# Performance work log

Measured on AMD Instinct MI355X. Metric: run time of the kernel, lower is better.

## Reference

```python
import jax, jax.numpy as jnp
import numpy as np
from jax import lax

B, T0, H0, W0 = 8, 8, 14, 14
C, NH = 768, 8
D = C // NH            # head_dim = 96
N = T0 * H0 * W0 + 1   # 1569 tokens incl. cls
SCALE = D ** -0.5
EPS = 1e-5


def _pool_norm(xh, conv_w, ln_g, ln_b, thw, stride):
    """AttentionPool with depthwise conv3d + LayerNorm. xh: [B, NH, N, D]."""
    cls_tok, xs = xh[:, :, :1, :], xh[:, :, 1:, :]
    b, n, _, d = xs.shape
    t, h, w = thw
    # (b n) c t h w
    xs = xs.reshape(b * n, t, h, w, d).transpose(0, 4, 1, 2, 3)
    y = lax.conv_general_dilated(
        xs, conv_w, window_strides=stride,
        padding=[(1, 1), (1, 1), (1, 1)],
        feature_group_count=d,
        dimension_numbers=("NCDHW", "OIDHW", "NCDHW"))
    ot, oh, ow = y.shape[2], y.shape[3], y.shape[4]
    y = y.transpose(0, 2, 3, 4, 1).reshape(b, n, ot * oh * ow, d)
    y = jnp.concatenate([cls_tok, y], axis=2)
    mu = y.mean(-1, keepdims=True)
    var = y.var(-1, keepdims=True)
    y = (y - mu) * lax.rsqrt(var + EPS) * ln_g + ln_b
    return y, (ot, oh, ow)


def setup_inputs() -> dict:
    key = jax.random.key(0)
    ks = jax.random.split(key, 12)
    s = lambda fan: (1.0 / np.sqrt(fan))
    return {
        "x": jax.random.normal(ks[0], (B, N, C), jnp.float32),
        "W_qkv": jax.random.normal(ks[1], (C, 3 * C), jnp.float32) * s(C),
        "b_qkv": jnp.zeros((3 * C,), jnp.float32),
        "W_proj": jax.random.normal(ks[2], (C, C), jnp.float32) * s(C),
        "b_proj": jnp.zeros((C,), jnp.float32),
        "conv_q_w": jax.random.normal(ks[3], (D, 1, 3, 3, 3), jnp.float32) * s(27),
        "conv_k_w": jax.random.normal(ks[4], (D, 1, 3, 3, 3), jnp.float32) * s(27),
        "conv_v_w": jax.random.normal(ks[5], (D, 1, 3, 3, 3), jnp.float32) * s(27),
        "lnq_g": jnp.ones((D,), jnp.float32), "lnq_b": jnp.zeros((D,), jnp.float32),
        "lnk_g": jnp.ones((D,), jnp.float32), "lnk_b": jnp.zeros((D,), jnp.float32),
        "lnv_g": jnp.ones((D,), jnp.float32), "lnv_b": jnp.zeros((D,), jnp.float32),
        "t": T0, "h": H0, "w": W0,
    }


def reference(x, W_qkv, b_qkv, W_proj, b_proj,
              conv_q_w, conv_k_w, conv_v_w,
              lnq_g, lnq_b, lnk_g, lnk_b, lnv_g, lnv_b,
              t, h, w):
    thw = (int(t), int(h), int(w))
    Bx, Nx, Cx = x.shape
    qkv = x @ W_qkv + b_qkv                       # [B, N, 3C]
    qkv = qkv.reshape(Bx, Nx, 3, NH, D).transpose(2, 0, 3, 1, 4)  # qkv b h n d
    q, k, v = qkv[0], qkv[1], qkv[2]
    q, q_shape = _pool_norm(q, conv_q_w, lnq_g, lnq_b, thw, (1, 1, 1))
    k, _ = _pool_norm(k, conv_k_w, lnk_g, lnk_b, thw, (1, 2, 2))
    v, _ = _pool_norm(v, conv_v_w, lnv_g, lnv_b, thw, (1, 2, 2))
    dots = jnp.einsum("bhid,bhjd->bhij", q, k) * SCALE
    attn = jax.nn.softmax(dots, axis=-1)
    out = jnp.einsum("bhij,bhjd->bhid", attn, v)  # [B, NH, Nq, D]
    out = out.transpose(0, 2, 1, 3).reshape(Bx, -1, Cx)
    out = out @ W_proj + b_proj
    return out
```

## Files before the change

### kernel.cpp

```cpp
#include <hip/hip_runtime.h>
#include <hip/hip_bf16.h>
#include <math.h>

#define B_   8
#define NH_  8
#define D_   96
#define C_   768
#define N_   1569
#define NKV_ 393
#define M_   (B_*N_)
#define QKV1 ((size_t)B_*NH_*N_*D_)
#define QPAD 1664
#define KPAD 416
#define SCALE_ 0.10206207261596575f

using short8v = __attribute__((ext_vector_type(8))) short;
using f32x4   = __attribute__((ext_vector_type(4))) float;
using f32x2   = __attribute__((ext_vector_type(2))) float;
typedef unsigned short u16;

#define GLOAD_LDS16(g, l) __builtin_amdgcn_global_load_lds( \
    (const __attribute__((address_space(1))) void*)(g),     \
    (__attribute__((address_space(3))) void*)(l), 16, 0, 0)

static __device__ __forceinline__ u16 f2bf(float f) {
    __hip_bfloat16 b = __float2bfloat16(f);
    return *(u16*)&b;
}

static __device__ __forceinline__ unsigned xcd_swizzle(unsigned orig, unsigned nwg) {
    const unsigned qq = nwg >> 3, rr = nwg & 7;
    const unsigned xcd = orig & 7, loc = orig >> 3;
    return (xcd < rr ? xcd * (qq + 1) : rr * (qq + 1) + (xcd - rr) * qq) + loc;
}

#define PREP_CVT_B   9414
#define PREP_WQ_B    1728
#define PREP_WP_B    576
#define PREP_WT_B    31
#define PREP_ZP_B    552
#define PREP_BLOCKS  (PREP_CVT_B + PREP_WQ_B + PREP_WP_B + PREP_WT_B + PREP_ZP_B)

static __device__ __forceinline__
void tile_transpose(const float* __restrict__ W, u16* __restrict__ Wt,
                    int ncols, int n0, int k0, float* tile )
{
    const int tx = threadIdx.x & 31, ty = threadIdx.x >> 5;
    #pragma unroll
    for (int i = 0; i < 4; ++i)
        tile[(ty + i * 8) * 33 + tx] = W[(size_t)(k0 + ty + i * 8) * ncols + n0 + tx];
    __syncthreads();
    #pragma unroll
    for (int i = 0; i < 4; ++i)
        Wt[(size_t)(n0 + ty + i * 8) * 768 + k0 + tx] = f2bf(tile[tx * 33 + ty + i * 8]);
}

__global__ __launch_bounds__(256)
void prep_kernel(const float* __restrict__ x, const float* __restrict__ Wqkv,
                 const float* __restrict__ Wproj,
                 const float* __restrict__ cwq, const float* __restrict__ cwk,
                 const float* __restrict__ cwv,
                 u16* __restrict__ x16, u16* __restrict__ Wqkvt,
                 u16* __restrict__ Wprojt, float* __restrict__ cwT,
                 u16* __restrict__ vt16)
{
    __shared__ float tile[32 * 33];
    const int bid = blockIdx.x;
    const int tid = threadIdx.x;

    if (bid < PREP_CVT_B) {
        const int i = bid * 256 + tid;
        const int n4 = M_ * 768 / 4;
        if (i < n4) {
            const float4 v = ((const float4*)x)[i];
            ushort4 o;
            o.x = f2bf(v.x); o.y = f2bf(v.y); o.z = f2bf(v.z); o.w = f2bf(v.w);
            ((ushort4*)x16)[i] = o;
        }
    } else if (bid < PREP_CVT_B + PREP_WQ_B) {
        const int b2 = bid - PREP_CVT_B;
        tile_transpose(Wqkv, Wqkvt, 2304, (b2 % 72) * 32, (b2 / 72) * 32, tile);
    } else if (bid < PREP_CVT_B + PREP_WQ_B + PREP_WP_B) {
        const int b2 = bid - PREP_CVT_B - PREP_WQ_B;
        tile_transpose(Wproj, Wprojt, 768, (b2 % 24) * 32, (b2 / 24) * 32, tile);
    } else if (bid < PREP_CVT_B + PREP_WQ_B + PREP_WP_B + PREP_WT_B) {
        const int i = (bid - PREP_CVT_B - PREP_WQ_B - PREP_WP_B) * 256 + tid;
        if (i < 3 * 27 * 96) {
            const int tsr = i / 2592;
            const int r = i - tsr * 2592;
            const int tap = r / 96, ch = r - tap * 96;
            const float* src = tsr == 0 ? cwq : (tsr == 1 ? cwk : cwv);
            cwT[i] = src[ch * 27 + tap];
        }
    } else {
        const int i = (bid - PREP_CVT_B - PREP_WQ_B - PREP_WP_B - PREP_WT_B) * 256 + tid;
        const int total = 64 * 96 * (KPAD - NKV_);
        if (i < total) {
            const int j = i % (KPAD - NKV_);
            const int rest = i / (KPAD - NKV_);
            vt16[(size_t)rest * KPAD + NKV_ + j] = 0;
        }
    }
}

template<int NC, bool SCATTER>
__global__ __launch_bounds__(512)
void gemm_bf16_kernel(const u16* __restrict__ A, const u16* __restrict__ Bt,
                      const float* __restrict__ bias, void* __restrict__ outp)
{
    constexpr int NXT = NC / 128;
    __shared__ alignas(16) u16 As[2][128 * 64];
    __shared__ alignas(16) u16 Bs[2][128 * 64];

    const int tid  = threadIdx.x;
    const int w    = tid >> 6, lane = tid & 63;
    const int c    = lane & 15, g = lane >> 4;
    const int wm   = w >> 2, wn = w & 3;
    const int lrow = lane >> 3, lcol = lane & 7;

    const unsigned wg = xcd_swizzle(blockIdx.x, gridDim.x);
    const int m0 = (int)(wg / NXT) * 128;
    const int n0 = (int)(wg % NXT) * 128;

    f32x4 acc[4][2];
    #pragma unroll
    for (int i = 0; i < 4; ++i)
        #pragma unroll
        for (int j = 0; j < 2; ++j) acc[i][j] = (f32x4){0.f, 0.f, 0.f, 0.f};

#define STAGE(BUF, K0) do {                                                      \
    _Pragma("unroll")                                                            \
    for (int t = 0; t < 2; ++t) {                                                \
        const int r = t * 64 + w * 8;                                            \
        const int row = r + lrow;                                                \
        const int scol = (lcol ^ (row & 7)) * 8;                                 \
        int m = m0 + row; if (m >= M_) m = M_ - 1;                               \
        GLOAD_LDS16(&A[(size_t)m * 768 + (K0) + scol], &As[BUF][r * 64]);        \
        GLOAD_LDS16(&Bt[(size_t)(n0 + row) * 768 + (K0) + scol],                 \
                    &Bs[BUF][r * 64]);                                           \
    } } while (0)

    const int xora = (g ^ (c & 7)) * 8;
    const int xorb = ((4 + g) ^ (c & 7)) * 8;

#define KSTEP(BUF, LAST, PREF, KNEXT) do {                                       \
    if (LAST) asm volatile("s_waitcnt vmcnt(0)" ::: "memory");                   \
    else      asm volatile("s_waitcnt vmcnt(4)" ::: "memory");                   \
    __builtin_amdgcn_s_barrier();                                                \
    short8v a0[4], a1[4], b0[2], b1[2];                                          \
    _Pragma("unroll")                                                            \
    for (int i = 0; i < 4; ++i) {                                                \
        const int ra = (wm * 64 + i * 16 + c) * 64;                              \
        a0[i] = *(const short8v*)&As[BUF][ra + xora];                            \
        a1[i] = *(const short8v*)&As[BUF][ra + xorb];                            \
    }                                                                            \
    _Pragma("unroll")                                                            \
    for (int j = 0; j < 2; ++j) {                                                \
        const int rb = (wn * 32 + j * 16 + c) * 64;                              \
        b0[j] = *(const short8v*)&Bs[BUF][rb + xora];                            \
        b1[j] = *(const short8v*)&Bs[BUF][rb + xorb];                            \
    }                                                                            \
    asm volatile("s_waitcnt lgkmcnt(0)" ::: "memory");                           \
    __builtin_amdgcn_sched_barrier(0);                                           \
    __builtin_amdgcn_s_barrier();                                                \
    if (PREF) STAGE(BUF, KNEXT);                                                 \
    __builtin_amdgcn_s_setprio(1);                                               \
    _Pragma("unroll")                                                            \
    for (int i = 0; i < 4; ++i)                                                  \
        _Pragma("unroll")                                                        \
        for (int j = 0; j < 2; ++j)                                              \
            acc[i][j] = __builtin_amdgcn_mfma_f32_16x16x32_bf16(                 \
                a0[i], b0[j], acc[i][j], 0, 0, 0);                               \
    _Pragma("unroll")                                                            \
    for (int i = 0; i < 4; ++i)                                                  \
        _Pragma("unroll")                                                        \
        for (int j = 0; j < 2; ++j)                                              \
            acc[i][j] = __builtin_amdgcn_mfma_f32_16x16x32_bf16(                 \
                a1[i], b1[j], acc[i][j], 0, 0, 0);                               \
    __builtin_amdgcn_s_setprio(0);                                               \
    } while (0)

    STAGE(0, 0);
    STAGE(1, 64);
    #pragma unroll
    for (int tt = 0; tt < 5; ++tt) {
        KSTEP(0, false, true, (2 * tt + 2) * 64);
        KSTEP(1, false, true, (2 * tt + 3) * 64);
    }
    KSTEP(0, false, false, 0);
    KSTEP(1, true,  false, 0);
#undef STAGE
#undef KSTEP

    #pragma unroll
    for (int i = 0; i < 4; ++i) {
        const int mrow = m0 + wm * 64 + i * 16 + g * 4;
        #pragma unroll
        for (int j = 0; j < 2; ++j) {
            const int ncol = n0 + wn * 32 + j * 16 + c;
            const float bv = bias[ncol];
            if constexpr (SCATTER) {
                u16* out = (u16*)outp;
                const int s   = ncol / C_;
                const int rem = ncol - s * C_;
                const int hh  = rem / D_;
                const int dd  = rem - hh * D_;
                #pragma unroll
                for (int r = 0; r < 4; ++r) {
                    const int m = mrow + r;
                    if (m < M_) {
                        const int bb2 = m / N_;
                        const int n = m - bb2 * N_;
                        out[(size_t)s * QKV1 +
                            ((size_t)(bb2 * NH_ + hh) * N_ + n) * D_ + dd] = f2bf(acc[i][j][r] + bv);
                    }
                }
            } else {
                float* out = (float*)outp;
                #pragma unroll
                for (int r = 0; r < 4; ++r) {
                    const int m = mrow + r;
                    if (m < M_) out[(size_t)m * NC + ncol] = acc[i][j][r] + bv;
                }
            }
        }
    }
}

static __device__ __forceinline__ void loadx6(const u16* __restrict__ rowp,
                                              int iw, f32x2 x[3])
{
    if (iw < 0 || iw >= 14) {
        x[0] = x[1] = x[2] = (f32x2){0.f, 0.f};
        return;
    }
    const unsigned* p = (const unsigned*)(rowp + (size_t)iw * 96);
    #pragma unroll
    for (int j = 0; j < 3; ++j) {
        const unsigned u = p[j];
        x[j][0] = __uint_as_float(u << 16);
        x[j][1] = __uint_as_float(u & 0xffff0000u);
    }
}

template<int STRIDE, int OHW, int WMODE, int WO0>
static __device__ __forceinline__
void pool_task(const u16* __restrict__ in, const float* __restrict__ cwT,
               const float* __restrict__ g, const float* __restrict__ bta,
               u16* __restrict__ out, int tokstride, int bh, int to, int ho,
               float oscale)
{
    const int sl = threadIdx.x & 15;
    const u16* base = in + (size_t)bh * N_ * 96 + 6 * sl;

    f32x2 acc[7][3];
    #pragma unroll
    for (int i = 0; i < 7; ++i)
        #pragma unroll
        for (int p = 0; p < 3; ++p) acc[i][p] = (f32x2){0.f, 0.f};

    #pragma unroll
    for (int dt = 0; dt < 3; ++dt) {
        const int t = to - 1 + dt;
        if (t < 0 || t > 7) continue;
        #pragma unroll
        for (int dh = 0; dh < 3; ++dh) {
            const int h = ho * STRIDE - 1 + dh;
            if (h < 0 || h >= 14) continue;
            const int tapb = dt * 9 + dh * 3;
            f32x2 wt[3][3];
            #pragma unroll
            for (int dw = 0; dw < 3; ++dw)
                #pragma unroll
                for (int p = 0; p < 3; ++p)
                    wt[dw][p] = *(const f32x2*)&cwT[(tapb + dw) * 96 + 6 * sl + 2 * p];
            const u16* rowp = base + (size_t)(1 + t * 196 + h * 14) * 96;

            if constexpr (STRIDE == 1) {
                f32x2 xm[3], x0[3], xp[3];
                loadx6(rowp, WO0 - 1, xm);
                loadx6(rowp, WO0, x0);
                #pragma unroll
                for (int wo = 0; wo < 7; ++wo) {
                    loadx6(rowp, WO0 + wo + 1, xp);
                    #pragma unroll
                    for (int p = 0; p < 3; ++p) {
                        acc[wo][p] = __builtin_elementwise_fma(wt[0][p], xm[p], acc[wo][p]);
                        acc[wo][p] = __builtin_elementwise_fma(wt[1][p], x0[p], acc[wo][p]);
                        acc[wo][p] = __builtin_elementwise_fma(wt[2][p], xp[p], acc[wo][p]);
                        xm[p] = x0[p]; x0[p] = xp[p];
                    }
                }
            } else {
                #pragma unroll
                for (int wo = 0; wo < 7; ++wo) {
                    #pragma unroll
                    for (int dw = 0; dw < 3; ++dw) {
                        f32x2 xa[3];
                        loadx6(rowp, 2 * wo - 1 + dw, xa);
                        #pragma unroll
                        for (int p = 0; p < 3; ++p)
                            acc[wo][p] = __builtin_elementwise_fma(wt[dw][p], xa[p], acc[wo][p]);
                    }
                }
            }
        }
    }

    f32x2 gg[3], bb[3];
    #pragma unroll
    for (int p = 0; p < 3; ++p) {
        gg[p] = *(const f32x2*)&g[6 * sl + 2 * p] * oscale;
        bb[p] = *(const f32x2*)&bta[6 * sl + 2 * p] * oscale;
    }

    #pragma unroll
    for (int wo = 0; wo < 7; ++wo) {
        float s = acc[wo][0][0] + acc[wo][0][1] + acc[wo][1][0] + acc[wo][1][1]
                + acc[wo][2][0] + acc[wo][2][1];
        float sq = acc[wo][0][0] * acc[wo][0][0];
        sq = fmaf(acc[wo][0][1], acc[wo][0][1], sq);
        sq = fmaf(acc[wo][1][0], acc[wo][1][0], sq);
        sq = fmaf(acc[wo][1][1], acc[wo][1][1], sq);
        sq = fmaf(acc[wo][2][0], acc[wo][2][0], sq);
        sq = fmaf(acc[wo][2][1], acc[wo][2][1], sq);
        #pragma unroll
        for (int off = 1; off < 16; off <<= 1) {
            s  += __shfl_xor(s, off, 64);
            sq += __shfl_xor(sq, off, 64);
        }
        const float mu = s * (1.f / 96.f);
        const float rstd = rsqrtf(sq * (1.f / 96.f) - mu * mu + 1e-5f);
        const f32x2 muv = (f32x2){mu, mu};
        const int tok = 1 + (to * OHW + ho) * OHW + WO0 + wo;
        u16 yb[6];
        #pragma unroll
        for (int p = 0; p < 3; ++p) {
            const f32x2 y = (acc[wo][p] - muv) * rstd * gg[p] + bb[p];
            yb[2 * p] = f2bf(y[0]); yb[2 * p + 1] = f2bf(y[1]);
        }
        if constexpr (WMODE == 2) {
            #pragma unroll
            for (int j = 0; j < 6; ++j)
                out[((size_t)bh * 96 + 6 * sl + j) * KPAD + tok] = yb[j];
        } else {
            unsigned* op = (unsigned*)&out[((size_t)bh * tokstride + tok) * 96 + 6 * sl];
            #pragma unroll
            for (int p = 0; p < 3; ++p)
                op[p] = (unsigned)yb[2 * p] | ((unsigned)yb[2 * p + 1] << 16);
        }
    }
}

template<int WMODE>
static __device__ __forceinline__
void pool_cls_v5(const u16* __restrict__ in, const float* __restrict__ g,
                 const float* __restrict__ bta, u16* __restrict__ out,
                 int tokstride, int bh, float oscale)
{
    const int sl = threadIdx.x & 15;
    const unsigned* p = (const unsigned*)(in + (size_t)bh * N_ * 96 + 6 * sl);
    f32x2 v[3];
    #pragma unroll
    for (int j = 0; j < 3; ++j) {
        const unsigned u = p[j];
        v[j][0] = __uint_as_float(u << 16);
        v[j][1] = __uint_as_float(u & 0xffff0000u);
    }
    float s = v[0][0] + v[0][1] + v[1][0] + v[1][1] + v[2][0] + v[2][1];
    float sq = v[0][0]*v[0][0] + v[0][1]*v[0][1] + v[1][0]*v[1][0]
             + v[1][1]*v[1][1] + v[2][0]*v[2][0] + v[2][1]*v[2][1];
    #pragma unroll
    for (int off = 1; off < 16; off <<= 1) {
        s  += __shfl_xor(s, off, 64);
        sq += __shfl_xor(sq, off, 64);
    }
    const float mu = s * (1.f / 96.f);
    const float rstd = rsqrtf(sq * (1.f / 96.f) - mu * mu + 1e-5f);
    u16 yb[6];
    #pragma unroll
    for (int p2 = 0; p2 < 3; ++p2) {
        const f32x2 gg = *(const f32x2*)&g[6 * sl + 2 * p2] * oscale;
        const f32x2 bb = *(const f32x2*)&bta[6 * sl + 2 * p2] * oscale;
        const f32x2 y = (v[p2] - (f32x2){mu, mu}) * rstd * gg + bb;
        yb[2 * p2] = f2bf(y[0]); yb[2 * p2 + 1] = f2bf(y[1]);
    }
    if constexpr (WMODE == 2) {
        #pragma unroll
        for (int j = 0; j < 6; ++j)
            out[((size_t)bh * 96 + 6 * sl + j) * KPAD] = yb[j];
    } else {
        unsigned* op = (unsigned*)&out[(size_t)bh * tokstride * 96 + 6 * sl];
        #pragma unroll
        for (int p2 = 0; p2 < 3; ++p2)
            op[p2] = (unsigned)yb[2 * p2] | ((unsigned)yb[2 * p2 + 1] << 16);
    }
}

#define NTASKS 21696
__global__ __launch_bounds__(256)
void pool_ln_v5_kernel(const u16* __restrict__ qin, const u16* __restrict__ kin,
                       const u16* __restrict__ vin, const float* __restrict__ cwT,
                       const float* __restrict__ gq, const float* __restrict__ bq,
                       const float* __restrict__ gk, const float* __restrict__ bk,
                       const float* __restrict__ gv, const float* __restrict__ bv,
                       u16* __restrict__ qout, u16* __restrict__ kout,
                       u16* __restrict__ vtout)
{
    const unsigned wg = xcd_swizzle(blockIdx.x, gridDim.x);
    const int gid = (int)(wg * 16 + (threadIdx.x >> 4));
    if (gid >= NTASKS) return;

    if (gid < 14336) {
        const int chunk = gid / 7168;
        const int r = gid - chunk * 7168;
        const int ho = r % 14;
        const int to = (r / 14) & 7;
        const int bh = r / 112;
        if (chunk == 0)
            pool_task<1, 14, 0, 0>(qin, cwT, gq, bq, qout, QPAD, bh, to, ho, SCALE_);
        else
            pool_task<1, 14, 0, 7>(qin, cwT, gq, bq, qout, QPAD, bh, to, ho, SCALE_);
    } else if (gid < 17920) {
        const int r = gid - 14336;
        const int ho = r % 7;
        const int to = (r / 7) & 7;
        const int bh = r / 56;
        pool_task<2, 7, 0, 0>(kin, cwT + 2592, gk, bk, kout, KPAD, bh, to, ho, 1.f);
    } else if (gid < 21504) {
        const int r = gid - 17920;
        const int ho = r % 7;
        const int to = (r / 7) & 7;
        const int bh = r / 56;
        pool_task<2, 7, 2, 0>(vin, cwT + 5184, gv, bv, vtout, KPAD, bh, to, ho, 1.f);
    } else {
        const int r = gid - 21504;
        const int tsr = r >> 6, bh = r & 63;
        if (tsr == 0)      pool_cls_v5<0>(qin, gq, bq, qout, QPAD, bh, SCALE_);
        else if (tsr == 1) pool_cls_v5<0>(kin, gk, bk, kout, KPAD, bh, 1.f);
        else               pool_cls_v5<2>(vin, gv, bv, vtout, KPAD, bh, 1.f);
    }
}

__global__ __launch_bounds__(256)
void attn_mfma_kernel(const u16* __restrict__ Q, const u16* __restrict__ K,
                      const u16* __restrict__ VT, u16* __restrict__ Out)
{
    __shared__ alignas(16) u16 plds[4][2][512];
    const int tid  = threadIdx.x;
    const int w    = tid >> 6, lane = tid & 63;
    const int c    = lane & 15, g = lane >> 4;

    const unsigned wg = xcd_swizzle(blockIdx.x, gridDim.x);
    const int bh = (int)(wg / 13);
    const int b  = bh >> 3, hh = bh & 7;
    const int q0 = (int)(wg % 13) * 128 + w * 32;

    const size_t qbase = (size_t)bh * QPAD * 96;
    const size_t kbase = (size_t)bh * KPAD * 96;

    short8v qa[2][3];
    #pragma unroll
    for (int s2 = 0; s2 < 2; ++s2)
        #pragma unroll
        for (int kf = 0; kf < 3; ++kf)
            qa[s2][kf] = *(const short8v*)
                &Q[qbase + (size_t)(q0 + s2 * 16 + c) * 96 + kf * 32 + g * 8];

    f32x4 oacc[2][6];
    #pragma unroll
    for (int s2 = 0; s2 < 2; ++s2)
        #pragma unroll
        for (int t = 0; t < 6; ++t) oacc[s2][t] = (f32x4){0.f, 0.f, 0.f, 0.f};
    float lsum[2][4] = {{0.f,0.f,0.f,0.f},{0.f,0.f,0.f,0.f}};

    short8v kb[2][6];
#define LOADK(IDX, PR) do {                                                     \
    _Pragma("unroll")                                                           \
    for (int h = 0; h < 2; ++h)                                                 \
        _Pragma("unroll")                                                       \
        for (int kf = 0; kf < 3; ++kf)                                          \
            kb[IDX][h * 3 + kf] = *(const short8v*)                             \
                &K[kbase + (size_t)((PR) * 32 + h * 16 + c) * 96 + kf * 32 + g * 8]; \
    } while (0)

    LOADK(0, 0);

    #pragma unroll
    for (int pr = 0; pr < 13; ++pr) {
        const int cur = pr & 1, nxt = cur ^ 1;

        short8v vt[6];
        #pragma unroll
        for (int t = 0; t < 6; ++t)
            vt[t] = *(const short8v*)
                &VT[kbase + (size_t)(t * 16 + c) * KPAD + pr * 32 + g * 8];

        f32x4 sacc[2][2];
        __builtin_amdgcn_s_setprio(1);
        #pragma unroll
        for (int s2 = 0; s2 < 2; ++s2)
            #pragma unroll
            for (int h = 0; h < 2; ++h) {
                f32x4 sa = (f32x4){0.f, 0.f, 0.f, 0.f};
                sa = __builtin_amdgcn_mfma_f32_16x16x32_bf16(qa[s2][0], kb[cur][h*3+0], sa, 0, 0, 0);
                sa = __builtin_amdgcn_mfma_f32_16x16x32_bf16(qa[s2][1], kb[cur][h*3+1], sa, 0, 0, 0);
                sa = __builtin_amdgcn_mfma_f32_16x16x32_bf16(qa[s2][2], kb[cur][h*3+2], sa, 0, 0, 0);
                sacc[s2][h] = sa;
            }
        __builtin_amdgcn_s_setprio(0);

        if (pr < 12) LOADK(nxt, pr + 1);

        #pragma unroll
        for (int h = 0; h < 2; ++h) {
            const int jcol = pr * 32 + h * 16 + c;
            #pragma unroll
            for (int r = 0; r < 4; ++r) {
                float s = sacc[0][h][r];
                if (jcol >= NKV_) s = -1e30f;
                const float p = __expf(s);
                lsum[0][r] += p;
                const int q    = g * 4 + r;
                const int j    = h * 16 + c;
                const int dstL = q | ((j >> 3) << 4);
                plds[w][0][dstL * 8 + (j & 7)] = f2bf(p);
            }
        }
        asm volatile("s_waitcnt lgkmcnt(0)" ::: "memory");
        __builtin_amdgcn_sched_barrier(0);
        {
            const short8v pa0 = *(const short8v*)&plds[w][0][lane * 8];
            __builtin_amdgcn_s_setprio(1);
            #pragma unroll
            for (int t = 0; t < 6; ++t)
                oacc[0][t] = __builtin_amdgcn_mfma_f32_16x16x32_bf16(pa0, vt[t], oacc[0][t], 0, 0, 0);
            __builtin_amdgcn_s_setprio(0);
        }

        #pragma unroll
        for (int h = 0; h < 2; ++h) {
            const int jcol = pr * 32 + h * 16 + c;
            #pragma unroll
            for (int r = 0; r < 4; ++r) {
                float s = sacc[1][h][r];
                if (jcol >= NKV_) s = -1e30f;
                const float p = __expf(s);
                lsum[1][r] += p;
                const int q    = g * 4 + r;
                const int j    = h * 16 + c;
                const int dstL = q | ((j >> 3) << 4);
                plds[w][1][dstL * 8 + (j & 7)] = f2bf(p);
            }
        }
        asm volatile("s_waitcnt lgkmcnt(0)" ::: "memory");
        __builtin_amdgcn_sched_barrier(0);
        {
            const short8v pa1 = *(const short8v*)&plds[w][1][lane * 8];
            __builtin_amdgcn_s_setprio(1);
            #pragma unroll
            for (int t = 0; t < 6; ++t)
                oacc[1][t] = __builtin_amdgcn_mfma_f32_16x16x32_bf16(pa1, vt[t], oacc[1][t], 0, 0, 0);
            __builtin_amdgcn_s_setprio(0);
        }
    }
#undef LOADK

    float linv[2][4];
    #pragma unroll
    for (int s2 = 0; s2 < 2; ++s2)
        #pragma unroll
        for (int r = 0; r < 4; ++r) {
            float s = lsum[s2][r];
            s += __shfl_xor(s, 1, 64);
            s += __shfl_xor(s, 2, 64);
            s += __shfl_xor(s, 4, 64);
            s += __shfl_xor(s, 8, 64);
            linv[s2][r] = 1.f / s;
        }

    #pragma unroll
    for (int s2 = 0; s2 < 2; ++s2)
        #pragma unroll
        for (int t = 0; t < 6; ++t)
            #pragma unroll
            for (int r = 0; r < 4; ++r) {
                const int row = q0 + s2 * 16 + g * 4 + r;
                if (row < N_)
                    Out[((size_t)(b * N_ + row)) * 768 + hh * 96 + t * 16 + c] =
                        f2bf(oacc[s2][t][r] * linv[s2][r]);
            }
}

extern "C" void kernel_launch(void* const* d_in, const int* in_sizes, int n_in,
                              void* d_out, int out_size, void* d_ws, size_t ws_size,
                              hipStream_t stream)
{
    const float* x     = (const float*)d_in[0];
    const float* Wqkv  = (const float*)d_in[1];
    const float* bqkv  = (const float*)d_in[2];
    const float* Wproj = (const float*)d_in[3];
    const float* bproj = (const float*)d_in[4];
    const float* cwq   = (const float*)d_in[5];
    const float* cwk   = (const float*)d_in[6];
    const float* cwv   = (const float*)d_in[7];
    const float* lnqg  = (const float*)d_in[8];
    const float* lnqb  = (const float*)d_in[9];
    const float* lnkg  = (const float*)d_in[10];
    const float* lnkb  = (const float*)d_in[11];
    const float* lnvg  = (const float*)d_in[12];
    const float* lnvb  = (const float*)d_in[13];

    u16* ws = (u16*)d_ws;
    u16* qkv_raw = ws;
    u16* q16 = qkv_raw + 3 * QKV1;
    u16* k16 = q16 + (size_t)64 * QPAD * 96;
    u16* vt16 = k16 + (size_t)64 * KPAD * 96;
    u16* x16    = vt16 + (size_t)64 * KPAD * 96;
    u16* Wqkvt  = x16 + (size_t)M_ * 768;
    u16* Wprojt = Wqkvt + (size_t)2304 * 768;
    float* cwT  = (float*)(Wprojt + (size_t)768 * 768);
    u16* attn16 = qkv_raw;
    float* out = (float*)d_out;

    prep_kernel<<<PREP_BLOCKS, 256, 0, stream>>>(
        x, Wqkv, Wproj, cwq, cwk, cwv, x16, Wqkvt, Wprojt, cwT, vt16);

    gemm_bf16_kernel<2304, true><<<18 * 99, 512, 0, stream>>>(x16, Wqkvt, bqkv, qkv_raw);

    pool_ln_v5_kernel<<<(NTASKS + 15) / 16, 256, 0, stream>>>(
        qkv_raw, qkv_raw + QKV1, qkv_raw + 2 * QKV1, cwT,
        lnqg, lnqb, lnkg, lnkb, lnvg, lnvb, q16, k16, vt16);

    attn_mfma_kernel<<<13 * 64, 256, 0, stream>>>(q16, k16, vt16, attn16);

    gemm_bf16_kernel<768, false><<<6 * 99, 512, 0, stream>>>(attn16, Wprojt, bproj, out);
}
```

Baseline: 199.2 us.

## Widen GEMM tile to 128x256 with single-buffered LDS

Both GEMMs now use 128x256 output tiles instead of 128x128, so each wave computes a 64x64 sub-tile with 16 accumulators, halving the grid size. The LDS double buffer is dropped in favour of a single buffer. The next K-slice is prefetched after the first half-step's reads and a full vmcnt(0) wait precedes each step. This aims to raise arithmetic intensity and cut A-tile reloads, at the cost of exposed load latency, more registers, and fewer blocks (297 for the projection GEMM), which may underfill the GPU.

Result: faster. 190.0 us (-4.6%).

```diff
diff --git a/kernel.cpp b/kernel.cpp
--- a/kernel.cpp
+++ b/kernel.cpp
@@ -104,13 +104,13 @@
 }
 
 template<int NC, bool SCATTER>
-__global__ __launch_bounds__(512)
+__global__ __launch_bounds__(512, 4)
 void gemm_bf16_kernel(const u16* __restrict__ A, const u16* __restrict__ Bt,
                       const float* __restrict__ bias, void* __restrict__ outp)
 {
-    constexpr int NXT = NC / 128;
-    __shared__ alignas(16) u16 As[2][128 * 64];
-    __shared__ alignas(16) u16 Bs[2][128 * 64];
+    constexpr int NXT = NC / 256;
+    __shared__ alignas(16) u16 As[128 * 64];
+    __shared__ alignas(16) u16 Bs[256 * 64];
 
     const int tid  = threadIdx.x;
     const int w    = tid >> 6, lane = tid & 63;
@@ -120,75 +120,81 @@
 
     const unsigned wg = xcd_swizzle(blockIdx.x, gridDim.x);
     const int m0 = (int)(wg / NXT) * 128;
-    const int n0 = (int)(wg % NXT) * 128;
-
-    f32x4 acc[4][2];
+    const int n0 = (int)(wg % NXT) * 256;
+
+    f32x4 acc[4][4];
     #pragma unroll
     for (int i = 0; i < 4; ++i)
         #pragma unroll
-        for (int j = 0; j < 2; ++j) acc[i][j] = (f32x4){0.f, 0.f, 0.f, 0.f};
-
-#define STAGE(BUF, K0) do {                                                      \
+        for (int j = 0; j < 4; ++j) acc[i][j] = (f32x4){0.f, 0.f, 0.f, 0.f};
+
+#define STAGE(K0) do {                                                           \
     _Pragma("unroll")                                                            \
-    for (int t = 0; t < 2; ++t) {                                                \
-        const int r = t * 64 + w * 8;                                            \
-        const int row = r + lrow;                                                \
+    for (int it2 = 0; it2 < 2; ++it2) {                                          \
+        const int rb = it2 * 64 + w * 8;                                         \
+        const int row = rb + lrow;                                               \
         const int scol = (lcol ^ (row & 7)) * 8;                                 \
         int m = m0 + row; if (m >= M_) m = M_ - 1;                               \
-        GLOAD_LDS16(&A[(size_t)m * 768 + (K0) + scol], &As[BUF][r * 64]);        \
-        GLOAD_LDS16(&Bt[(size_t)(n0 + row) * 768 + (K0) + scol],                 \
-                    &Bs[BUF][r * 64]);                                           \
+        GLOAD_LDS16(&A[(size_t)m * 768 + (K0) + scol], &As[rb * 64]);            \
+    }                                                                            \
+    _Pragma("unroll")                                                            \
+    for (int it2 = 0; it2 < 4; ++it2) {                                          \
+        const int rb = it2 * 64 + w * 8;                                         \
+        const int row = rb + lrow;                                               \
+        const int scol = (lcol ^ (row & 7)) * 8;                                 \
+        GLOAD_LDS16(&Bt[(size_t)(n0 + row) * 768 + (K0) + scol], &Bs[rb * 64]);  \
     } } while (0)
 
     const int xora = (g ^ (c & 7)) * 8;
     const int xorb = ((4 + g) ^ (c & 7)) * 8;
 
-#define KSTEP(BUF, LAST, PREF, KNEXT) do {                                       \
-    if (LAST) asm volatile("s_waitcnt vmcnt(0)" ::: "memory");                   \
-    else      asm volatile("s_waitcnt vmcnt(4)" ::: "memory");                   \
+#define KSTEP(T) do {                                                            \
+    asm volatile("s_waitcnt vmcnt(0)" ::: "memory");                             \
     __builtin_amdgcn_s_barrier();                                                \
-    short8v a0[4], a1[4], b0[2], b1[2];                                          \
-    _Pragma("unroll")                                                            \
-    for (int i = 0; i < 4; ++i) {                                                \
-        const int ra = (wm * 64 + i * 16 + c) * 64;                              \
-        a0[i] = *(const short8v*)&As[BUF][ra + xora];                            \
-        a1[i] = *(const short8v*)&As[BUF][ra + xorb];                            \
+    {                                                                            \
+        short8v a0[4], b0[4];                                                    \
+        _Pragma("unroll")                                                        \
+        for (int i = 0; i < 4; ++i)                                              \
+            a0[i] = *(const short8v*)&As[(wm * 64 + i * 16 + c) * 64 + xora];    \
+        _Pragma("unroll")                                                        \
+        for (int j = 0; j < 4; ++j)                                              \
+            b0[j] = *(const short8v*)&Bs[(wn * 64 + j * 16 + c) * 64 + xora];    \
+        asm volatile("s_waitcnt lgkmcnt(0)" ::: "memory");                       \
+        __builtin_amdgcn_sched_barrier(0);                                       \
+        __builtin_amdgcn_s_setprio(1);                                           \
+        _Pragma("unroll")                                                        \
+        for (int i = 0; i < 4; ++i)                                              \
+            _Pragma("unroll")                                                    \
+            for (int j = 0; j < 4; ++j)                                          \
+                acc[i][j] = __builtin_amdgcn_mfma_f32_16x16x32_bf16(             \
+                    a0[i], b0[j], acc[i][j], 0, 0, 0);                           \
+        __builtin_amdgcn_s_setprio(0);                                           \
     }                                                                            \
-    _Pragma("unroll")                                                            \
-    for (int j = 0; j < 2; ++j) {                                                \
-        const int rb = (wn * 32 + j * 16 + c) * 64;                              \
-        b0[j] = *(const short8v*)&Bs[BUF][rb + xora];                            \
-        b1[j] = *(const short8v*)&Bs[BUF][rb + xorb];                            \
-    }                                                                            \
-    asm volatile("s_waitcnt lgkmcnt(0)" ::: "memory");                           \
-    __builtin_amdgcn_sched_barrier(0);                                           \
-    __builtin_amdgcn_s_barrier();                                                \
-    if (PREF) STAGE(BUF, KNEXT);                                                 \
-    __builtin_amdgcn_s_setprio(1);                                               \
-    _Pragma("unroll")                                                            \
-    for (int i = 0; i < 4; ++i)                                                  \
+    {                                                                            \
+        short8v a1[4], b1[4];                                                    \
         _Pragma("unroll")                                                        \
-        for (int j = 0; j < 2; ++j)                                              \
-            acc[i][j] = __builtin_amdgcn_mfma_f32_16x16x32_bf16(                 \
-                a0[i], b0[j], acc[i][j], 0, 0, 0);                               \
-    _Pragma("unroll")                                                            \
-    for (int i = 0; i < 4; ++i)                                                  \
+        for (int i = 0; i < 4; ++i)                                              \
+            a1[i] = *(const short8v*)&As[(wm * 64 + i * 16 + c) * 64 + xorb];    \
         _Pragma("unroll")                                                        \
-        for (int j = 0; j < 2; ++j)                                              \
-            acc[i][j] = __builtin_amdgcn_mfma_f32_16x16x32_bf16(                 \
-                a1[i], b1[j], acc[i][j], 0, 0, 0);                               \
-    __builtin_amdgcn_s_setprio(0);                                               \
-    } while (0)
-
-    STAGE(0, 0);
-    STAGE(1, 64);
-    #pragma unroll
-    for (int tt = 0; tt < 5; ++tt) {
-        KSTEP(0, false, true, (2 * tt + 2) * 64);
-        KSTEP(1, false, true, (2 * tt + 3) * 64);
-    }
-    KSTEP(0, false, false, 0);
-    KSTEP(1, true,  false, 0);
+        for (int j = 0; j < 4; ++j)                                              \
+            b1[j] = *(const short8v*)&Bs[(wn * 64 + j * 16 + c) * 64 + xorb];    \
+        asm volatile("s_waitcnt lgkmcnt(0)" ::: "memory");                       \
+        __builtin_amdgcn_sched_barrier(0);                                       \
+        __builtin_amdgcn_s_barrier();                                            \
+        if ((T) + 1 < 12) STAGE(((T) + 1) * 64);                                 \
+        __builtin_amdgcn_s_setprio(1);                                           \
+        _Pragma("unroll")                                                        \
+        for (int i = 0; i < 4; ++i)                                              \
+            _Pragma("unroll")                                                    \
+            for (int j = 0; j < 4; ++j)                                          \
+                acc[i][j] = __builtin_amdgcn_mfma_f32_16x16x32_bf16(             \
+                    a1[i], b1[j], acc[i][j], 0, 0, 0);                           \
+        __builtin_amdgcn_s_setprio(0);                                           \
+    } } while (0)
+
+    STAGE(0);
+    #pragma unroll
+    for (int t = 0; t < 12; ++t) KSTEP(t);
 #undef STAGE
 #undef KSTEP
 
@@ -196,8 +202,8 @@
     for (int i = 0; i < 4; ++i) {
         const int mrow = m0 + wm * 64 + i * 16 + g * 4;
         #pragma unroll
-        for (int j = 0; j < 2; ++j) {
-            const int ncol = n0 + wn * 32 + j * 16 + c;
+        for (int j = 0; j < 4; ++j) {
+            const int ncol = n0 + wn * 64 + j * 16 + c;
             const float bv = bias[ncol];
             if constexpr (SCATTER) {
                 u16* out = (u16*)outp;
@@ -626,7 +632,7 @@
     prep_kernel<<<PREP_BLOCKS, 256, 0, stream>>>(
         x, Wqkv, Wproj, cwq, cwk, cwv, x16, Wqkvt, Wprojt, cwT, vt16);
 
-    gemm_bf16_kernel<2304, true><<<18 * 99, 512, 0, stream>>>(x16, Wqkvt, bqkv, qkv_raw);
+    gemm_bf16_kernel<2304, true><<<99 * 9, 512, 0, stream>>>(x16, Wqkvt, bqkv, qkv_raw);
 
     pool_ln_v5_kernel<<<(NTASKS + 15) / 16, 256, 0, stream>>>(
         qkv_raw, qkv_raw + QKV1, qkv_raw + 2 * QKV1, cwT,
@@ -634,5 +640,5 @@
 
     attn_mfma_kernel<<<13 * 64, 256, 0, stream>>>(q16, k16, vt16, attn16);
 
-    gemm_bf16_kernel<768, false><<<6 * 99, 512, 0, stream>>>(attn16, Wprojt, bproj, out);
-}
+    gemm_bf16_kernel<768, false><<<99 * 3, 512, 0, stream>>>(attn16, Wprojt, bproj, out);
+}
```

## Single-buffer GEMM LDS with split-phase prefetch and wider N tile for QKV

Applied to the files above, without the earlier changes.

Restructures the bf16 GEMM from a double-buffered LDS pipeline to a single buffer. The next K-tile load is issued mid-step, after the fragment reads into registers, and overlaps with the second half of the MFMAs. It also adds a templated N tile, so the QKV projection uses 256-wide tiles with half as many blocks, and sets a launch-bounds occupancy hint. The aim is to cut LDS footprint for higher occupancy and to reuse A tiles across more columns, at the cost of extra barriers and less prefetch distance per step.

Result: slower. 298.9 us (+50.1%).

```diff
diff --git a/kernel.cpp b/kernel.cpp
--- a/kernel.cpp
+++ b/kernel.cpp
@@ -103,14 +103,21 @@
     }
 }
 
-template<int NC, bool SCATTER>
-__global__ __launch_bounds__(512)
+#define WAIT_VM(n)  asm volatile("s_waitcnt vmcnt(" #n ")" ::: "memory")
+#define WAIT_LG(n)  asm volatile("s_waitcnt lgkmcnt(" #n ")" ::: "memory")
+
+template<int NC, int BN, bool SCATTER>
+__global__ __launch_bounds__(512, 4)
 void gemm_bf16_kernel(const u16* __restrict__ A, const u16* __restrict__ Bt,
                       const float* __restrict__ bias, void* __restrict__ outp)
 {
-    constexpr int NXT = NC / 128;
-    __shared__ alignas(16) u16 As[2][128 * 64];
-    __shared__ alignas(16) u16 Bs[2][128 * 64];
+    constexpr int NXT    = NC / BN;
+    constexpr int WN     = BN / 4;
+    constexpr int NBF    = WN / 16;
+    constexpr int BLOADS = BN / 64;
+
+    __shared__ alignas(16) u16 As[128 * 64];
+    __shared__ alignas(16) u16 Bs[BN * 64];
 
     const int tid  = threadIdx.x;
     const int w    = tid >> 6, lane = tid & 63;
@@ -120,75 +127,81 @@
 
     const unsigned wg = xcd_swizzle(blockIdx.x, gridDim.x);
     const int m0 = (int)(wg / NXT) * 128;
-    const int n0 = (int)(wg % NXT) * 128;
-
-    f32x4 acc[4][2];
+    const int n0 = (int)(wg % NXT) * BN;
+
+    f32x4 acc[4][NBF];
     #pragma unroll
     for (int i = 0; i < 4; ++i)
         #pragma unroll
-        for (int j = 0; j < 2; ++j) acc[i][j] = (f32x4){0.f, 0.f, 0.f, 0.f};
-
-#define STAGE(BUF, K0) do {                                                      \
+        for (int j = 0; j < NBF; ++j) acc[i][j] = (f32x4){0.f, 0.f, 0.f, 0.f};
+
+#define STAGE(K0) do {                                                           \
     _Pragma("unroll")                                                            \
-    for (int t = 0; t < 2; ++t) {                                                \
-        const int r = t * 64 + w * 8;                                            \
-        const int row = r + lrow;                                                \
+    for (int it2 = 0; it2 < 2; ++it2) {                                          \
+        const int rb = it2 * 64 + w * 8;                                         \
+        const int row = rb + lrow;                                               \
         const int scol = (lcol ^ (row & 7)) * 8;                                 \
         int m = m0 + row; if (m >= M_) m = M_ - 1;                               \
-        GLOAD_LDS16(&A[(size_t)m * 768 + (K0) + scol], &As[BUF][r * 64]);        \
-        GLOAD_LDS16(&Bt[(size_t)(n0 + row) * 768 + (K0) + scol],                 \
-                    &Bs[BUF][r * 64]);                                           \
+        GLOAD_LDS16(&A[(size_t)m * 768 + (K0) + scol], &As[rb * 64]);            \
+    }                                                                            \
+    _Pragma("unroll")                                                            \
+    for (int it2 = 0; it2 < BLOADS; ++it2) {                                     \
+        const int rb = it2 * 64 + w * 8;                                         \
+        const int row = rb + lrow;                                               \
+        const int scol = (lcol ^ (row & 7)) * 8;                                 \
+        GLOAD_LDS16(&Bt[(size_t)(n0 + row) * 768 + (K0) + scol], &Bs[rb * 64]);  \
     } } while (0)
 
     const int xora = (g ^ (c & 7)) * 8;
     const int xorb = ((4 + g) ^ (c & 7)) * 8;
 
-#define KSTEP(BUF, LAST, PREF, KNEXT) do {                                       \
-    if (LAST) asm volatile("s_waitcnt vmcnt(0)" ::: "memory");                   \
-    else      asm volatile("s_waitcnt vmcnt(4)" ::: "memory");                   \
+#define KSTEP(T) do {                                                            \
+          \
+    if constexpr (BLOADS == 4) WAIT_VM(4); else WAIT_VM(2);                      \
     __builtin_amdgcn_s_barrier();                                                \
-    short8v a0[4], a1[4], b0[2], b1[2];                                          \
+    short8v a0[4], a1[4], b0[NBF], b1[NBF];                                      \
     _Pragma("unroll")                                                            \
     for (int i = 0; i < 4; ++i) {                                                \
         const int ra = (wm * 64 + i * 16 + c) * 64;                              \
-        a0[i] = *(const short8v*)&As[BUF][ra + xora];                            \
-        a1[i] = *(const short8v*)&As[BUF][ra + xorb];                            \
+        a0[i] = *(const short8v*)&As[ra + xora];                                 \
+        a1[i] = *(const short8v*)&As[ra + xorb];                                 \
     }                                                                            \
+                                  \
+    WAIT_VM(0);                                                                  \
+    __builtin_amdgcn_s_barrier();                                                \
     _Pragma("unroll")                                                            \
-    for (int j = 0; j < 2; ++j) {                                                \
-        const int rb = (wn * 32 + j * 16 + c) * 64;                              \
-        b0[j] = *(const short8v*)&Bs[BUF][rb + xora];                            \
-        b1[j] = *(const short8v*)&Bs[BUF][rb + xorb];                            \
+    for (int j = 0; j < NBF; ++j) {                                              \
+        const int rb = (wn * WN + j * 16 + c) * 64;                              \
+        b0[j] = *(const short8v*)&Bs[rb + xora];                                 \
+        b1[j] = *(const short8v*)&Bs[rb + xorb];                                 \
     }                                                                            \
-    asm volatile("s_waitcnt lgkmcnt(0)" ::: "memory");                           \
+    if constexpr (NBF == 4) WAIT_LG(4); else WAIT_LG(2);                         \
     __builtin_amdgcn_sched_barrier(0);                                           \
-    __builtin_amdgcn_s_barrier();                                                \
-    if (PREF) STAGE(BUF, KNEXT);                                                 \
     __builtin_amdgcn_s_setprio(1);                                               \
     _Pragma("unroll")                                                            \
     for (int i = 0; i < 4; ++i)                                                  \
         _Pragma("unroll")                                                        \
-        for (int j = 0; j < 2; ++j)                                              \
+        for (int j = 0; j < NBF; ++j)                                            \
             acc[i][j] = __builtin_amdgcn_mfma_f32_16x16x32_bf16(                 \
                 a0[i], b0[j], acc[i][j], 0, 0, 0);                               \
+    __builtin_amdgcn_s_setprio(0);                                               \
+    WAIT_LG(0);                                                                  \
+    __builtin_amdgcn_sched_barrier(0);                                           \
+    __builtin_amdgcn_s_barrier();                                                \
+    if ((T) + 1 < 12) STAGE(((T) + 1) * 64);                                     \
+    __builtin_amdgcn_s_setprio(1);                                               \
     _Pragma("unroll")                                                            \
     for (int i = 0; i < 4; ++i)                                                  \
         _Pragma("unroll")                                                        \
-        for (int j = 0; j < 2; ++j)                                              \
+        for (int j = 0; j < NBF; ++j)                                            \
             acc[i][j] = __builtin_amdgcn_mfma_f32_16x16x32_bf16(                 \
                 a1[i], b1[j], acc[i][j], 0, 0, 0);                               \
     __builtin_amdgcn_s_setprio(0);                                               \
     } while (0)
 
-    STAGE(0, 0);
-    STAGE(1, 64);
-    #pragma unroll
-    for (int tt = 0; tt < 5; ++tt) {
-        KSTEP(0, false, true, (2 * tt + 2) * 64);
-        KSTEP(1, false, true, (2 * tt + 3) * 64);
-    }
-    KSTEP(0, false, false, 0);
-    KSTEP(1, true,  false, 0);
+    STAGE(0);
+    #pragma unroll
+    for (int t = 0; t < 12; ++t) KSTEP(t);
 #undef STAGE
 #undef KSTEP
 
@@ -196,8 +209,8 @@
     for (int i = 0; i < 4; ++i) {
         const int mrow = m0 + wm * 64 + i * 16 + g * 4;
         #pragma unroll
-        for (int j = 0; j < 2; ++j) {
-            const int ncol = n0 + wn * 32 + j * 16 + c;
+        for (int j = 0; j < NBF; ++j) {
+            const int ncol = n0 + wn * WN + j * 16 + c;
             const float bv = bias[ncol];
             if constexpr (SCATTER) {
                 u16* out = (u16*)outp;
@@ -626,7 +639,7 @@
     prep_kernel<<<PREP_BLOCKS, 256, 0, stream>>>(
         x, Wqkv, Wproj, cwq, cwk, cwv, x16, Wqkvt, Wprojt, cwT, vt16);
 
-    gemm_bf16_kernel<2304, true><<<18 * 99, 512, 0, stream>>>(x16, Wqkvt, bqkv, qkv_raw);
+    gemm_bf16_kernel<2304, 256, true><<<99 * 9, 512, 0, stream>>>(x16, Wqkvt, bqkv, qkv_raw);
 
     pool_ln_v5_kernel<<<(NTASKS + 15) / 16, 256, 0, stream>>>(
         qkv_raw, qkv_raw + QKV1, qkv_raw + 2 * QKV1, cwT,
@@ -634,5 +647,5 @@
 
     attn_mfma_kernel<<<13 * 64, 256, 0, stream>>>(q16, k16, vt16, attn16);
 
-    gemm_bf16_kernel<768, false><<<6 * 99, 512, 0, stream>>>(attn16, Wprojt, bproj, out);
-}
+    gemm_bf16_kernel<768, 128, false><<<99 * 6, 512, 0, stream>>>(attn16, Wprojt, bproj, out);
+}
```
